# Optimization experiments

Measured on AMD Instinct MI355X. Metric: run time of the kernel, lower is better.

Reference implementation:

```python
import jax, jax.numpy as jnp
import numpy as np

B, S, D = 2, 2048, 256
H, C = 8, 32          # headNum, cDim (D == H*C)
OUT = 256             # outDim
WIN = 32              # localWindowSize (half-width)
NEG = -1e30


def setup_inputs() -> dict:
    key = jax.random.key(0)
    ks = jax.random.split(key, 9)
    scale_qk = 1.0 / np.sqrt(D)
    return {
        "Qin": jax.random.normal(ks[0], (B, S, D), jnp.float32),
        "Kin": jax.random.normal(ks[1], (B, S, D), jnp.float32),
        "Vin": jax.random.normal(ks[2], (B, S, D), jnp.float32),
        "QTrans": jax.random.normal(ks[3], (D, H * C), jnp.float32) * scale_qk,
        "KTrans": jax.random.normal(ks[4], (D, H * C), jnp.float32) * scale_qk,
        "VTrans": jax.random.normal(ks[5], (D, H * C), jnp.float32) * scale_qk,
        "GW": jax.random.normal(ks[6], (H * C, D), jnp.float32) * scale_qk,  # nn.Linear weight [out,in]
        "Gb": jnp.ones((H * C,), jnp.float32),
        "OW": jax.random.normal(ks[7], (OUT, H * C), jnp.float32) * scale_qk,
        "Ob": jnp.zeros((OUT,), jnp.float32),
    }


def reference(Qin, Kin, Vin, QTrans, KTrans, VTrans, GW, Gb, OW, Ob):
    b, s, _ = Qin.shape
    # projections -> [b, s, H, C]
    Q = (Qin @ QTrans).reshape(b, s, H, C)
    K = (Kin @ KTrans).reshape(b, s, H, C)
    V = (Vin @ VTrans).reshape(b, s, H, C)
    G = jax.nn.sigmoid(Vin @ GW.T + Gb).reshape(b, s, H, C)

    # dense scores [b, H, s, t] (matches original hnst layout with batch/head swapped)
    A = jnp.einsum('bshc,bthc->bhst', Q, K) / jnp.sqrt(jnp.asarray(C, Q.dtype))

    # whose index clamping only re-hits in-window edge positions)
    idx = jnp.arange(s)
    local = jnp.abs(idx[:, None] - idx[None, :]) <= WIN  # [s, s]
    A = jnp.where(local[None, None, :, :], A, NEG)

    A = jax.nn.softmax(A, axis=-1)

    # gated attention output: original einsum 'hnst,hnti,hnsi->nshi'
    O = jnp.einsum('bhst,bthc,bshc->bshc', A, V, G)
    return O.reshape(b, s, H * C) @ OW.T + Ob
```

## Files before the change

### kernel.cpp

```cpp
#include <hip/hip_runtime.h>
#include <hip/hip_bf16.h>

typedef __bf16 bf16_t;
typedef __attribute__((ext_vector_type(8))) __bf16 bf16x8;
typedef __attribute__((ext_vector_type(4))) __bf16 bf16x4;
typedef __attribute__((ext_vector_type(4))) float f32x4;

#define MFMA(a, b, c) __builtin_amdgcn_mfma_f32_16x16x32_bf16((a), (b), (c), 0, 0, 0)

#define WK 260

static __device__ __forceinline__ bf16x8 zero_bf16x8() {
  bf16x8 z;
#pragma unroll
  for (int i = 0; i < 8; ++i) z[i] = (bf16_t)0.f;
  return z;
}

static __device__ __forceinline__ bf16x8 join8(bf16x4 lo, bf16x4 hi) {
  bf16x8 r;
  r[0] = lo[0]; r[1] = lo[1]; r[2] = lo[2]; r[3] = lo[3];
  r[4] = hi[0]; r[5] = hi[1]; r[6] = hi[2]; r[7] = hi[3];
  return r;
}

static __device__ __forceinline__ bf16x8 cvt8(float4 a, float4 b) {
  bf16x8 r;
  r[0] = (bf16_t)a.x; r[1] = (bf16_t)a.y; r[2] = (bf16_t)a.z; r[3] = (bf16_t)a.w;
  r[4] = (bf16_t)b.x; r[5] = (bf16_t)b.y; r[6] = (bf16_t)b.z; r[7] = (bf16_t)b.w;
  return r;
}

__global__ __launch_bounds__(256) void proj_kernel(
    const float* __restrict__ Qin, const float* __restrict__ Kin,
    const float* __restrict__ Vin, const float* __restrict__ QT,
    const float* __restrict__ KT, const float* __restrict__ VTr,
    const float* __restrict__ GW, const float* __restrict__ Gb,
    bf16_t* __restrict__ Qb, bf16_t* __restrict__ Kb,
    bf16_t* __restrict__ VT, bf16_t* __restrict__ G) {
  __shared__ bf16_t Wl[64][WK];
  const int tid = threadIdx.x, w = tid >> 6, lane = tid & 63;
  const int quad = lane >> 4, t15 = lane & 15;
  const int job = blockIdx.z;
  const int m0 = blockIdx.x * 128 + w * 16;
  const int n0 = blockIdx.y * 64;
  const float* A = (job == 0) ? Qin : (job == 1) ? Kin : Vin;

  if (job < 3) {
    const float* src = (job == 0) ? QT : (job == 1) ? KT : VTr;
    const int nl = tid & 63;
    const int kq = (tid >> 6) * 4;
#pragma unroll
    for (int i = 0; i < 16; ++i) {
      int k0 = i * 16 + kq;
      float f0 = src[(size_t)(k0 + 0) * 256 + n0 + nl];
      float f1 = src[(size_t)(k0 + 1) * 256 + n0 + nl];
      float f2 = src[(size_t)(k0 + 2) * 256 + n0 + nl];
      float f3 = src[(size_t)(k0 + 3) * 256 + n0 + nl];
      bf16x4 w4;
      w4[0] = (bf16_t)f0; w4[1] = (bf16_t)f1; w4[2] = (bf16_t)f2; w4[3] = (bf16_t)f3;
      *(bf16x4*)&Wl[nl][k0] = w4;
    }
  } else {
    const int kk = (tid & 63) * 4;
    const int nw = tid >> 6;
#pragma unroll
    for (int i = 0; i < 16; ++i) {
      int n = i * 4 + nw;
      float4 v = *(const float4*)(GW + (size_t)(n0 + n) * 256 + kk);
      bf16x4 w4;
      w4[0] = (bf16_t)v.x; w4[1] = (bf16_t)v.y; w4[2] = (bf16_t)v.z; w4[3] = (bf16_t)v.w;
      *(bf16x4*)&Wl[n][kk] = w4;
    }
  }
  __syncthreads();

  const f32x4 zf = {0.f, 0.f, 0.f, 0.f};
  f32x4 acc[2][4] = {{zf, zf, zf, zf}, {zf, zf, zf, zf}};

  for (int kc = 0; kc < 8; ++kc) {
    bf16x8 a[2];
#pragma unroll
    for (int mi = 0; mi < 2; ++mi) {
      const float* ap = A + (size_t)(m0 + mi * 64 + t15) * 256 + kc * 32 + quad * 8;
      float4 x0 = *(const float4*)ap;
      float4 x1 = *(const float4*)(ap + 4);
      a[mi] = cvt8(x0, x1);
    }
#pragma unroll
    for (int nf = 0; nf < 4; ++nf) {
      bf16x4 lo = *(const bf16x4*)&Wl[nf * 16 + t15][kc * 32 + quad * 8];
      bf16x4 hi = *(const bf16x4*)&Wl[nf * 16 + t15][kc * 32 + quad * 8 + 4];
      bf16x8 bw = join8(lo, hi);
#pragma unroll
      for (int mi = 0; mi < 2; ++mi) acc[mi][nf] = MFMA(a[mi], bw, acc[mi][nf]);
    }
  }

#pragma unroll
  for (int mi = 0; mi < 2; ++mi) {
    const int mm0 = m0 + mi * 64 + quad * 4;
    if (job == 2) {
      const int b = mm0 >> 11;
      const int s = mm0 & 2047;
#pragma unroll
      for (int nf = 0; nf < 4; ++nf) {
        int nn = n0 + nf * 16 + t15;
        int h = nn >> 5, c = nn & 31;
        bf16x4 v4;
#pragma unroll
        for (int r = 0; r < 4; ++r) v4[r] = (bf16_t)acc[mi][nf][r];
        *(bf16x4*)(VT + (size_t)((b * 8 + h) * 32 + c) * 2048 + s) = v4;
      }
    } else if (job == 3) {
#pragma unroll
      for (int nf = 0; nf < 4; ++nf) {
        int nn = n0 + nf * 16 + t15;
        float bias = Gb[nn];
#pragma unroll
        for (int r = 0; r < 4; ++r) {
          float g = 1.f / (1.f + __expf(-(acc[mi][nf][r] + bias)));
          G[(size_t)(mm0 + r) * 256 + nn] = (bf16_t)g;
        }
      }
    } else {
      bf16_t* dst = (job == 0) ? Qb : Kb;
#pragma unroll
      for (int nf = 0; nf < 4; ++nf) {
        int nn = n0 + nf * 16 + t15;
#pragma unroll
        for (int r = 0; r < 4; ++r)
          dst[(size_t)(mm0 + r) * 256 + nn] = (bf16_t)acc[mi][nf][r];
      }
    }
  }
}

__global__ __launch_bounds__(512) void attn_out_kernel(
    const bf16_t* __restrict__ Qb, const bf16_t* __restrict__ Kb,
    const bf16_t* __restrict__ VT, const bf16_t* __restrict__ G,
    const float* __restrict__ OW, const float* __restrict__ Ob,
    float* __restrict__ out) {
  __shared__ bf16_t P[8][16][104];
  __shared__ bf16_t Ol[16][WK];
  const int tid = threadIdx.x, h = tid >> 6, lane = tid & 63;
  const int quad = lane >> 4, t15 = lane & 15;
  const int qt = blockIdx.x & 127, b = blockIdx.x >> 7;
  const int q0 = qt * 16, tbase = q0 - 32;
  const size_t rowbase = (size_t)b * 2048;

  bf16x8 aq = *(const bf16x8*)(Qb + (rowbase + q0 + t15) * 256 + h * 32 + quad * 8);

  float g0[4], g1[4];
#pragma unroll
  for (int r = 0; r < 4; ++r) {
    size_t base = (rowbase + q0 + quad * 4 + r) * 256 + h * 32;
    g0[r] = (float)G[base + t15];
    g1[r] = (float)G[base + 16 + t15];
  }
  const float ob0 = Ob[h * 32 + t15];
  const float ob1 = Ob[h * 32 + 16 + t15];

  const f32x4 zf = {0.f, 0.f, 0.f, 0.f};
  f32x4 sc[5];
#pragma unroll
  for (int j = 0; j < 5; ++j) {
    int t = tbase + j * 16 + t15;
    bf16x8 bk = zero_bf16x8();
    if ((unsigned)t < 2048u)
      bk = *(const bf16x8*)(Kb + (rowbase + t) * 256 + h * 32 + quad * 8);
    sc[j] = MFMA(aq, bk, zf);
  }

  const float scale = 0.17677669529663687f;
  float mx[4] = {-3.0e38f, -3.0e38f, -3.0e38f, -3.0e38f};
#pragma unroll
  for (int j = 0; j < 5; ++j) {
    int t = tbase + j * 16 + t15;
#pragma unroll
    for (int r = 0; r < 4; ++r) {
      int q = q0 + quad * 4 + r;
      int dd = q - t;
      bool valid = ((unsigned)t < 2048u) && (dd <= 32) && (dd >= -32);
      float v = valid ? sc[j][r] * scale : -1e30f;
      sc[j][r] = v;
      mx[r] = fmaxf(mx[r], v);
    }
  }
#pragma unroll
  for (int off = 1; off < 16; off <<= 1) {
#pragma unroll
    for (int r = 0; r < 4; ++r) mx[r] = fmaxf(mx[r], __shfl_xor(mx[r], off));
  }
  float sum[4] = {0.f, 0.f, 0.f, 0.f};
#pragma unroll
  for (int j = 0; j < 5; ++j) {
#pragma unroll
    for (int r = 0; r < 4; ++r) {
      float e = __expf(sc[j][r] - mx[r]);
      sc[j][r] = e;
      sum[r] += e;
    }
  }
#pragma unroll
  for (int off = 1; off < 16; off <<= 1) {
#pragma unroll
    for (int r = 0; r < 4; ++r) sum[r] += __shfl_xor(sum[r], off);
  }
  float inv[4];
#pragma unroll
  for (int r = 0; r < 4; ++r) inv[r] = 1.f / sum[r];

#pragma unroll
  for (int j = 0; j < 5; ++j) {
#pragma unroll
    for (int r = 0; r < 4; ++r)
      P[h][quad * 4 + r][j * 16 + t15] = (bf16_t)(sc[j][r] * inv[r]);
  }
#pragma unroll
  for (int r = 0; r < 4; ++r) P[h][quad * 4 + r][80 + t15] = (bf16_t)0.f;
  __syncthreads();

  f32x4 y0 = zf, y1 = zf;
#pragma unroll
  for (int kc = 0; kc < 3; ++kc) {
    bf16x8 pa = *(const bf16x8*)&P[h][t15][kc * 32 + quad * 8];
    int ts = tbase + kc * 32 + quad * 8;
    bf16x8 bv0 = zero_bf16x8(), bv1 = zero_bf16x8();
    if (ts >= 0 && ts + 8 <= 2048) {
      const bf16_t* vbase = VT + ((size_t)((b * 8 + h) * 32) + t15) * 2048 + ts;
      bv0 = *(const bf16x8*)vbase;
      bv1 = *(const bf16x8*)(vbase + (size_t)16 * 2048);
    }
    y0 = MFMA(pa, bv0, y0);
    y1 = MFMA(pa, bv1, y1);
  }

#pragma unroll
  for (int r = 0; r < 4; ++r) {
    Ol[quad * 4 + r][h * 32 + t15] = (bf16_t)(y0[r] * g0[r]);
    Ol[quad * 4 + r][h * 32 + 16 + t15] = (bf16_t)(y1[r] * g1[r]);
  }
  __syncthreads();

  f32x4 acc[2] = {zf, zf};
  for (int kc = 0; kc < 8; ++kc) {
    bf16x4 alo = *(const bf16x4*)&Ol[t15][kc * 32 + quad * 8];
    bf16x4 ahi = *(const bf16x4*)&Ol[t15][kc * 32 + quad * 8 + 4];
    bf16x8 a = join8(alo, ahi);
#pragma unroll
    for (int nf = 0; nf < 2; ++nf) {
      int n = h * 32 + nf * 16 + t15;
      const float* wp = OW + (size_t)n * 256 + kc * 32 + quad * 8;
      float4 w0 = *(const float4*)wp;
      float4 w1 = *(const float4*)(wp + 4);
      acc[nf] = MFMA(a, cvt8(w0, w1), acc[nf]);
    }
  }
#pragma unroll
  for (int nf = 0; nf < 2; ++nf) {
    int n = h * 32 + nf * 16 + t15;
    float bias = (nf == 0) ? ob0 : ob1;
#pragma unroll
    for (int r = 0; r < 4; ++r)
      out[(rowbase + q0 + quad * 4 + r) * 256 + n] = acc[nf][r] + bias;
  }
}

extern "C" void kernel_launch(void* const* d_in, const int* in_sizes, int n_in,
                              void* d_out, int out_size, void* d_ws, size_t ws_size,
                              hipStream_t stream) {
  const float* Qin = (const float*)d_in[0];
  const float* Kin = (const float*)d_in[1];
  const float* Vin = (const float*)d_in[2];
  const float* QT  = (const float*)d_in[3];
  const float* KT  = (const float*)d_in[4];
  const float* VTr = (const float*)d_in[5];
  const float* GW  = (const float*)d_in[6];
  const float* Gb  = (const float*)d_in[7];
  const float* OW  = (const float*)d_in[8];
  const float* Ob  = (const float*)d_in[9];
  float* out = (float*)d_out;

  char* ws = (char*)d_ws;
  const size_t MB = 1u << 20;
  bf16_t* Qb = (bf16_t*)(ws + 0 * MB);
  bf16_t* Kb = (bf16_t*)(ws + 2 * MB);
  bf16_t* VT = (bf16_t*)(ws + 4 * MB);
  bf16_t* G  = (bf16_t*)(ws + 6 * MB);

  proj_kernel<<<dim3(32, 4, 4), 256, 0, stream>>>(Qin, Kin, Vin, QT, KT, VTr,
                                                  GW, Gb, Qb, Kb, VT, G);
  attn_out_kernel<<<256, 512, 0, stream>>>(Qb, Kb, VT, G, OW, Ob, out);
}
```

Before: 102.4 us.

## Widen projection tiles, stage V transpose in LDS, pre-convert OW, prefetch V

The projection kernel now computes 128-column tiles instead of 64, halving the grid and the number of times each activation row is reloaded. The V projection output is transposed through shared memory so the VT stores become coalesced 16-byte writes. An extra job converts the output weight to bf16 once, so the attention kernel loads bf16 weights directly instead of converting fp32 on every use. The attention kernel also prefetches V fragments early, remaps block indices and unrolls the output GEMM loop. The cost is more registers and LDS per projection block and fewer blocks to spread across the GPU.

New measurement: 101.3 us. About the same (-1.0%).

```diff
diff --git a/kernel.cpp b/kernel.cpp
--- a/kernel.cpp
+++ b/kernel.cpp
@@ -36,23 +36,41 @@
     const float* __restrict__ Vin, const float* __restrict__ QT,
     const float* __restrict__ KT, const float* __restrict__ VTr,
     const float* __restrict__ GW, const float* __restrict__ Gb,
+    const float* __restrict__ OW,
     bf16_t* __restrict__ Qb, bf16_t* __restrict__ Kb,
-    bf16_t* __restrict__ VT, bf16_t* __restrict__ G) {
-  __shared__ bf16_t Wl[64][WK];
+    bf16_t* __restrict__ VT, bf16_t* __restrict__ G,
+    bf16_t* __restrict__ OWb) {
+  __shared__ bf16_t Wl[128][WK];
   const int tid = threadIdx.x, w = tid >> 6, lane = tid & 63;
   const int quad = lane >> 4, t15 = lane & 15;
   const int job = blockIdx.z;
+
+  if (job == 4) {
+    if (blockIdx.y != 0 || blockIdx.x >= 4) return;
+    const int base = blockIdx.x * 16384 + tid * 4;
+#pragma unroll
+    for (int i = 0; i < 16; ++i) {
+      int idx = base + i * 1024;
+      float4 v = *(const float4*)(OW + idx);
+      bf16x4 o;
+      o[0] = (bf16_t)v.x; o[1] = (bf16_t)v.y;
+      o[2] = (bf16_t)v.z; o[3] = (bf16_t)v.w;
+      *(bf16x4*)(OWb + idx) = o;
+    }
+    return;
+  }
+
   const int m0 = blockIdx.x * 128 + w * 16;
-  const int n0 = blockIdx.y * 64;
+  const int n0 = blockIdx.y * 128;
   const float* A = (job == 0) ? Qin : (job == 1) ? Kin : Vin;
 
   if (job < 3) {
     const float* src = (job == 0) ? QT : (job == 1) ? KT : VTr;
-    const int nl = tid & 63;
-    const int kq = (tid >> 6) * 4;
-#pragma unroll
-    for (int i = 0; i < 16; ++i) {
-      int k0 = i * 16 + kq;
+    const int nl = tid & 127;
+    const int kq = (tid >> 7) * 4;
+#pragma unroll 8
+    for (int i = 0; i < 32; ++i) {
+      int k0 = i * 8 + kq;
       float f0 = src[(size_t)(k0 + 0) * 256 + n0 + nl];
       float f1 = src[(size_t)(k0 + 1) * 256 + n0 + nl];
       float f2 = src[(size_t)(k0 + 2) * 256 + n0 + nl];
@@ -64,8 +82,8 @@
   } else {
     const int kk = (tid & 63) * 4;
     const int nw = tid >> 6;
-#pragma unroll
-    for (int i = 0; i < 16; ++i) {
+#pragma unroll 8
+    for (int i = 0; i < 32; ++i) {
       int n = i * 4 + nw;
       float4 v = *(const float4*)(GW + (size_t)(n0 + n) * 256 + kk);
       bf16x4 w4;
@@ -76,7 +94,11 @@
   __syncthreads();
 
   const f32x4 zf = {0.f, 0.f, 0.f, 0.f};
-  f32x4 acc[2][4] = {{zf, zf, zf, zf}, {zf, zf, zf, zf}};
+  f32x4 acc[2][8];
+#pragma unroll
+  for (int mi = 0; mi < 2; ++mi)
+#pragma unroll
+    for (int nf = 0; nf < 8; ++nf) acc[mi][nf] = zf;
 
   for (int kc = 0; kc < 8; ++kc) {
     bf16x8 a[2];
@@ -88,7 +110,7 @@
       a[mi] = cvt8(x0, x1);
     }
 #pragma unroll
-    for (int nf = 0; nf < 4; ++nf) {
+    for (int nf = 0; nf < 8; ++nf) {
       bf16x4 lo = *(const bf16x4*)&Wl[nf * 16 + t15][kc * 32 + quad * 8];
       bf16x4 hi = *(const bf16x4*)&Wl[nf * 16 + t15][kc * 32 + quad * 8 + 4];
       bf16x8 bw = join8(lo, hi);
@@ -97,24 +119,37 @@
     }
   }
 
-#pragma unroll
-  for (int mi = 0; mi < 2; ++mi) {
-    const int mm0 = m0 + mi * 64 + quad * 4;
-    if (job == 2) {
-      const int b = mm0 >> 11;
-      const int s = mm0 & 2047;
-#pragma unroll
-      for (int nf = 0; nf < 4; ++nf) {
-        int nn = n0 + nf * 16 + t15;
-        int h = nn >> 5, c = nn & 31;
-        bf16x4 v4;
-#pragma unroll
-        for (int r = 0; r < 4; ++r) v4[r] = (bf16_t)acc[mi][nf][r];
-        *(bf16x4*)(VT + (size_t)((b * 8 + h) * 32 + c) * 2048 + s) = v4;
+  if (job == 2) {
+    __syncthreads();
+    bf16_t* Sb = &Wl[0][0];
+#pragma unroll
+    for (int mi = 0; mi < 2; ++mi) {
+      const int m = mi * 64 + w * 16 + quad * 4;
+#pragma unroll
+      for (int nf = 0; nf < 8; ++nf) {
+        const int n = nf * 16 + t15;
+#pragma unroll
+        for (int r = 0; r < 4; ++r) Sb[n * 136 + m + r] = (bf16_t)acc[mi][nf][r];
       }
-    } else if (job == 3) {
-#pragma unroll
-      for (int nf = 0; nf < 4; ++nf) {
+    }
+    __syncthreads();
+    const int mloc = (tid & 15) * 8;
+    const int nl2 = tid >> 4;
+    const int mg = blockIdx.x * 128 + mloc;
+    const int bb = mg >> 11, s = mg & 2047;
+#pragma unroll
+    for (int p = 0; p < 8; ++p) {
+      const int ng = n0 + p * 16 + nl2;
+      const int hh = ng >> 5, c = ng & 31;
+      bf16x8 v = *(const bf16x8*)&Sb[(p * 16 + nl2) * 136 + mloc];
+      *(bf16x8*)(VT + (size_t)((bb * 8 + hh) * 32 + c) * 2048 + s) = v;
+    }
+  } else if (job == 3) {
+#pragma unroll
+    for (int mi = 0; mi < 2; ++mi) {
+      const int mm0 = m0 + mi * 64 + quad * 4;
+#pragma unroll
+      for (int nf = 0; nf < 8; ++nf) {
         int nn = n0 + nf * 16 + t15;
         float bias = Gb[nn];
 #pragma unroll
@@ -123,10 +158,14 @@
           G[(size_t)(mm0 + r) * 256 + nn] = (bf16_t)g;
         }
       }
-    } else {
-      bf16_t* dst = (job == 0) ? Qb : Kb;
-#pragma unroll
-      for (int nf = 0; nf < 4; ++nf) {
+    }
+  } else {
+    bf16_t* dst = (job == 0) ? Qb : Kb;
+#pragma unroll
+    for (int mi = 0; mi < 2; ++mi) {
+      const int mm0 = m0 + mi * 64 + quad * 4;
+#pragma unroll
+      for (int nf = 0; nf < 8; ++nf) {
         int nn = n0 + nf * 16 + t15;
 #pragma unroll
         for (int r = 0; r < 4; ++r)
@@ -139,17 +178,31 @@
 __global__ __launch_bounds__(512) void attn_out_kernel(
     const bf16_t* __restrict__ Qb, const bf16_t* __restrict__ Kb,
     const bf16_t* __restrict__ VT, const bf16_t* __restrict__ G,
-    const float* __restrict__ OW, const float* __restrict__ Ob,
+    const bf16_t* __restrict__ OWb, const float* __restrict__ Ob,
     float* __restrict__ out) {
   __shared__ bf16_t P[8][16][104];
   __shared__ bf16_t Ol[16][WK];
   const int tid = threadIdx.x, h = tid >> 6, lane = tid & 63;
   const int quad = lane >> 4, t15 = lane & 15;
-  const int qt = blockIdx.x & 127, b = blockIdx.x >> 7;
+  const int bid = ((blockIdx.x & 7) << 5) | (blockIdx.x >> 3);
+  const int qt = bid & 127, b = bid >> 7;
   const int q0 = qt * 16, tbase = q0 - 32;
   const size_t rowbase = (size_t)b * 2048;
 
   bf16x8 aq = *(const bf16x8*)(Qb + (rowbase + q0 + t15) * 256 + h * 32 + quad * 8);
+
+  bf16x8 bv[3][2];
+#pragma unroll
+  for (int kc = 0; kc < 3; ++kc) {
+    int ts = tbase + kc * 32 + quad * 8;
+    bv[kc][0] = zero_bf16x8();
+    bv[kc][1] = zero_bf16x8();
+    if (ts >= 0 && ts + 8 <= 2048) {
+      const bf16_t* vb = VT + ((size_t)((b * 8 + h) * 32) + t15) * 2048 + ts;
+      bv[kc][0] = *(const bf16x8*)vb;
+      bv[kc][1] = *(const bf16x8*)(vb + (size_t)16 * 2048);
+    }
+  }
 
   float g0[4], g1[4];
 #pragma unroll
@@ -225,15 +278,8 @@
 #pragma unroll
   for (int kc = 0; kc < 3; ++kc) {
     bf16x8 pa = *(const bf16x8*)&P[h][t15][kc * 32 + quad * 8];
-    int ts = tbase + kc * 32 + quad * 8;
-    bf16x8 bv0 = zero_bf16x8(), bv1 = zero_bf16x8();
-    if (ts >= 0 && ts + 8 <= 2048) {
-      const bf16_t* vbase = VT + ((size_t)((b * 8 + h) * 32) + t15) * 2048 + ts;
-      bv0 = *(const bf16x8*)vbase;
-      bv1 = *(const bf16x8*)(vbase + (size_t)16 * 2048);
-    }
-    y0 = MFMA(pa, bv0, y0);
-    y1 = MFMA(pa, bv1, y1);
+    y0 = MFMA(pa, bv[kc][0], y0);
+    y1 = MFMA(pa, bv[kc][1], y1);
   }
 
 #pragma unroll
@@ -244,6 +290,7 @@
   __syncthreads();
 
   f32x4 acc[2] = {zf, zf};
+#pragma unroll
   for (int kc = 0; kc < 8; ++kc) {
     bf16x4 alo = *(const bf16x4*)&Ol[t15][kc * 32 + quad * 8];
     bf16x4 ahi = *(const bf16x4*)&Ol[t15][kc * 32 + quad * 8 + 4];
@@ -251,10 +298,8 @@
 #pragma unroll
     for (int nf = 0; nf < 2; ++nf) {
       int n = h * 32 + nf * 16 + t15;
-      const float* wp = OW + (size_t)n * 256 + kc * 32 + quad * 8;
-      float4 w0 = *(const float4*)wp;
-      float4 w1 = *(const float4*)(wp + 4);
-      acc[nf] = MFMA(a, cvt8(w0, w1), acc[nf]);
+      bf16x8 w8 = *(const bf16x8*)(OWb + (size_t)n * 256 + kc * 32 + quad * 8);
+      acc[nf] = MFMA(a, w8, acc[nf]);
     }
   }
 #pragma unroll
@@ -284,12 +329,13 @@
 
   char* ws = (char*)d_ws;
   const size_t MB = 1u << 20;
-  bf16_t* Qb = (bf16_t*)(ws + 0 * MB);
-  bf16_t* Kb = (bf16_t*)(ws + 2 * MB);
-  bf16_t* VT = (bf16_t*)(ws + 4 * MB);
-  bf16_t* G  = (bf16_t*)(ws + 6 * MB);
-
-  proj_kernel<<<dim3(32, 4, 4), 256, 0, stream>>>(Qin, Kin, Vin, QT, KT, VTr,
-                                                  GW, Gb, Qb, Kb, VT, G);
-  attn_out_kernel<<<256, 512, 0, stream>>>(Qb, Kb, VT, G, OW, Ob, out);
-}
+  bf16_t* Qb  = (bf16_t*)(ws + 0 * MB);
+  bf16_t* Kb  = (bf16_t*)(ws + 2 * MB);
+  bf16_t* VT  = (bf16_t*)(ws + 4 * MB);
+  bf16_t* G   = (bf16_t*)(ws + 6 * MB);
+  bf16_t* OWb = (bf16_t*)(ws + 8 * MB);
+
+  proj_kernel<<<dim3(32, 2, 5), 256, 0, stream>>>(Qin, Kin, Vin, QT, KT, VTr,
+                                                  GW, Gb, OW, Qb, Kb, VT, G, OWb);
+  attn_out_kernel<<<256, 512, 0, stream>>>(Qb, Kb, VT, G, OWb, Ob, out);
+}
```
